# Performance work log

Hardware: AMD Instinct MI355X
Metric: run time of the kernel (lower is better)

The kernel has to match this reference:

```python
import jax, jax.numpy as jnp
import numpy as np

N = 8192      # atoms
F = 133       # atom feature length
H = 256       # hidden_size
MF = 200      # mol feature length
RH = 512      # readout_hidden_size
DEPTH = 3
N_RO = 2      # readout_num_hidden_layers
DEG = 32      # avg degree of random graph


def setup_inputs() -> dict:
    key = jax.random.key(0)
    ks = jax.random.split(key, 16)
    sc = 0.05
    adjacency_matrix = (jax.random.uniform(ks[0], (N, N)) < (DEG / N)).astype(jnp.float32)
    atom_feature_matrix = jax.random.normal(ks[1], (N, F), jnp.float32)
    molecule_features_vector = jax.random.normal(ks[2], (MF,), jnp.float32)
    return {
        "adjacency_matrix": adjacency_matrix,
        "atom_feature_matrix": atom_feature_matrix,
        "molecule_features_vector": molecule_features_vector,
        "W_in": jax.random.normal(ks[3], (F, H), jnp.float32) * sc,
        "b_in": jnp.zeros((H,), jnp.float32),
        "W_att": jax.random.normal(ks[4], (2 * H,), jnp.float32) * sc,
        "b_att": jnp.zeros((), jnp.float32),
        "W_node": jax.random.normal(ks[5], (DEPTH, H, H), jnp.float32) * sc,
        "b_node": jnp.zeros((DEPTH, H), jnp.float32),
        "W_ro_in": jax.random.normal(ks[6], (H + MF, RH), jnp.float32) * sc,
        "b_ro_in": jnp.zeros((RH,), jnp.float32),
        "W_ro_hid": jax.random.normal(ks[7], (N_RO, RH, RH), jnp.float32) * sc,
        "b_ro_hid": jnp.zeros((N_RO, RH), jnp.float32),
        "W_out": jax.random.normal(ks[8], (RH,), jnp.float32) * sc,
        "b_out": jnp.zeros((), jnp.float32),
    }


def reference(adjacency_matrix, atom_feature_matrix, molecule_features_vector,
              W_in, b_in, W_att, b_att, W_node, b_node,
              W_ro_in, b_ro_in, W_ro_hid, b_ro_hid, W_out, b_out):
    # input node-level linear
    h = atom_feature_matrix @ W_in + b_in                     # [N, H]
    wa_nei, wa_self = W_att[:H], W_att[H:]                    # concat([neighbor, self]) ordering
    for d in range(DEPTH):
        # attention score[i, j] = sigmoid(w_nei . h_j + w_self . h_i + b)
        s_nei = h @ wa_nei                                    # [N]
        s_self = h @ wa_self                                  # [N]
        att = jax.nn.sigmoid(s_self[:, None] + s_nei[None, :] + b_att)  # [N, N]
        # adjacency is binary: zeros stay zero, nonzeros get scaled by sigmoid score
        h = (adjacency_matrix * att) @ h                      # sum aggregation, [N, H]
        h = jax.nn.relu(h @ W_node[d] + b_node[d])
    # readout: sum over atoms, concat mol features
    g = jnp.sum(h, axis=0)                                    # [H]
    g = jnp.concatenate([g, molecule_features_vector])        # [H + MF]
    g = jax.nn.relu(g @ W_ro_in + b_ro_in)
    for d in range(N_RO):
        g = jax.nn.relu(g @ W_ro_hid[d] + b_ro_hid[d])
    return g @ W_out + b_out                                  # scalar
```

## Files before the change

### kernel.cpp

```cpp
#include <hip/hip_runtime.h>
#include <hip/hip_bf16.h>
#include <math.h>

#define N 8192
#define F 133
#define FP 136
#define H 256
#define MF 200
#define RH 512
#define MAXDEG 128

typedef unsigned short bfu;

static __device__ __forceinline__ bfu f2bf(float f) {
    unsigned u = __builtin_bit_cast(unsigned, f);
    u = (u + 0x7fff + ((u >> 16) & 1)) >> 16;
    return (bfu)u;
}
static __device__ __forceinline__ float bf2f(bfu b) {
    unsigned u = (unsigned)b << 16;
    return __builtin_bit_cast(float, u);
}

__global__ __launch_bounds__(256) void k_front(
    const float4* __restrict__ A4, int* __restrict__ cnt, int* __restrict__ colidx,
    const float* __restrict__ X, const float* __restrict__ Win,
    const float* __restrict__ bin, const float* __restrict__ Watt,
    bfu* __restrict__ hb, float* __restrict__ snei, float* __restrict__ sself,
    float* __restrict__ zbuf) {
    const int t = threadIdx.x;
    const int b = blockIdx.x;
    if (b == 2304) {
        for (int i = t; i < 1792; i += 256) zbuf[i] = 0.f;
        return;
    }
    if (b >= 256) {
        const int lane = t & 63;
        const int row = (b - 256) * 4 + (t >> 6);
        const float4* rowp = A4 + (size_t)row * (N / 4);
        unsigned w4[4];
#pragma unroll 1
        for (int c = 0; c < 4; ++c) {
            float4 v[8];
#pragma unroll
            for (int j = 0; j < 8; ++j) v[j] = rowp[c * 512 + j * 64 + lane];
            unsigned m = 0;
#pragma unroll
            for (int j = 0; j < 8; ++j) {
                const float* vp = &v[j].x;
#pragma unroll
                for (int q = 0; q < 4; ++q)
                    m |= (vp[q] != 0.0f) ? (1u << (j * 4 + q)) : 0u;
            }
            w4[c] = m;
        }
        int tl = __popc(w4[0]) + __popc(w4[1]) + __popc(w4[2]) + __popc(w4[3]);
        int inc = tl;
#pragma unroll
        for (int d = 1; d < 64; d <<= 1) {
            int nb = __shfl_up(inc, d);
            if (lane >= d) inc += nb;
        }
        int o = inc - tl;
        if (lane == 63) cnt[row] = inc < MAXDEG ? inc : MAXDEG;
        int* rowout = colidx + row * MAXDEG;
#pragma unroll
        for (int c = 0; c < 4; ++c) {
            unsigned m = w4[c];
            const int base = c * 2048 + lane * 4;
            while (m) {
                int p = __ffs(m) - 1;
                m &= m - 1;
                if (o < MAXDEG) rowout[o] = base + ((p >> 2) << 8) + (p & 3);
                ++o;
            }
        }
        return;
    }
    __shared__ float xs[32][FP];
    __shared__ float sredN[32][4];
    __shared__ float sredS[32][4];
    const int row0 = b * 32;
    for (int i = t; i < 32 * F; i += 256) {
        int r = i / F, f = i - r * F;
        xs[r][f] = X[(row0 + r) * F + f];
    }
    __syncthreads();
    float acc[32];
#pragma unroll
    for (int r = 0; r < 32; ++r) acc[r] = 0.f;
    for (int f = 0; f < 132; f += 4) {
        float w0 = Win[(f + 0) * H + t];
        float w1 = Win[(f + 1) * H + t];
        float w2 = Win[(f + 2) * H + t];
        float w3 = Win[(f + 3) * H + t];
#pragma unroll
        for (int r = 0; r < 32; ++r) {
            float4 xv = *reinterpret_cast<const float4*>(&xs[r][f]);
            acc[r] = fmaf(xv.x, w0, acc[r]);
            acc[r] = fmaf(xv.y, w1, acc[r]);
            acc[r] = fmaf(xv.z, w2, acc[r]);
            acc[r] = fmaf(xv.w, w3, acc[r]);
        }
    }
    {
        float w0 = Win[132 * H + t];
#pragma unroll
        for (int r = 0; r < 32; ++r) acc[r] = fmaf(xs[r][132], w0, acc[r]);
    }
    const float bb = bin[t];
    const float wan = Watt[t];
    const float was = Watt[H + t];
    const int wv = t >> 6, ln = t & 63;
#pragma unroll
    for (int r = 0; r < 32; ++r) {
        float v = acc[r] + bb;
        hb[(row0 + r) * H + t] = f2bf(v);
        float pn = v * wan;
        float ps = v * was;
        for (int off = 32; off > 0; off >>= 1) {
            pn += __shfl_down(pn, off);
            ps += __shfl_down(ps, off);
        }
        if (ln == 0) { sredN[r][wv] = pn; sredS[r][wv] = ps; }
    }
    __syncthreads();
    if (t < 32)
        snei[row0 + t] = (sredN[t][0] + sredN[t][1]) + (sredN[t][2] + sredN[t][3]);
    else if (t < 64) {
        int r = t - 32;
        sself[row0 + r] = (sredS[r][0] + sredS[r][1]) + (sredS[r][2] + sredS[r][3]);
    }
}

template <bool LAST>
__global__ __launch_bounds__(512, 2) void k_depth(
    const bfu* __restrict__ hin, bfu* __restrict__ hout,
    const int* __restrict__ cnt, const int* __restrict__ colidx,
    const float* __restrict__ snei_in, const float* __restrict__ sself_in,
    float* __restrict__ snei_out, float* __restrict__ sself_out,
    const float* __restrict__ Wn, const float* __restrict__ bn,
    const float* __restrict__ Watt, const float* __restrict__ b_att,
    float* __restrict__ gsum) {
    __shared__ float hs[32][260];
    __shared__ float uni[8192];
    __shared__ float sred[8 * 256];
    __shared__ float sselfL[32];
    __shared__ int   ncnt[32];
    const int t = threadIdx.x;
    const int w = t >> 6, l = t & 63;
    const int c0 = l << 2;
    const int R0 = blockIdx.x * 32;
    float* wls = uni;
    unsigned short* jls = (unsigned short*)(uni + 4096);

    if (t < 32) { ncnt[t] = cnt[R0 + t]; sselfL[t] = sself_in[R0 + t] + b_att[0]; }
    __syncthreads();
#pragma unroll
    for (int rep = 0; rep < 8; ++rep) {
        int idx = t + rep * 512;
        int r = idx >> 7, k = idx & 127;
        if (k < ncnt[r]) {
            int j = colidx[(R0 + r) * MAXDEG + k];
            jls[idx] = (unsigned short)j;
            wls[idx] = 1.f / (1.f + __expf(-(sselfL[r] + snei_in[j])));
        }
    }
    __syncthreads();
#define GSTEP(u, sx, sy, sz, sw)                                                  \
    { int ju = (int)jls[r * 128 + k + u]; float wv = wls[r * 128 + k + u];        \
      ushort4 hv = *reinterpret_cast<const ushort4*>(&hin[ju * 256 + c0]);        \
      sx = fmaf(wv, bf2f(hv.x), sx); sy = fmaf(wv, bf2f(hv.y), sy);               \
      sz = fmaf(wv, bf2f(hv.z), sz); sw = fmaf(wv, bf2f(hv.w), sw); }
#pragma unroll 1
    for (int rr = 0; rr < 4; ++rr) {
        const int r = w * 4 + rr;
        const int n = ncnt[r];
        float x0=0,y0=0,z0=0,w0=0, x1=0,y1=0,z1=0,w1=0;
        float x2=0,y2=0,z2=0,w2=0, x3=0,y3=0,z3=0,w3=0;
        float x4=0,y4=0,z4=0,w4=0, x5=0,y5=0,z5=0,w5=0;
        float x6=0,y6=0,z6=0,w6=0, x7=0,y7=0,z7=0,w7=0;
        int k = 0;
        for (; k + 8 <= n; k += 8) {
            GSTEP(0,x0,y0,z0,w0) GSTEP(1,x1,y1,z1,w1)
            GSTEP(2,x2,y2,z2,w2) GSTEP(3,x3,y3,z3,w3)
            GSTEP(4,x4,y4,z4,w4) GSTEP(5,x5,y5,z5,w5)
            GSTEP(6,x6,y6,z6,w6) GSTEP(7,x7,y7,z7,w7)
        }
        for (; k < n; ++k) { GSTEP(0,x0,y0,z0,w0) }
        float4 st;
        st.x = ((x0+x1)+(x2+x3)) + ((x4+x5)+(x6+x7));
        st.y = ((y0+y1)+(y2+y3)) + ((y4+y5)+(y6+y7));
        st.z = ((z0+z1)+(z2+z3)) + ((z4+z5)+(z6+z7));
        st.w = ((w0+w1)+(w2+w3)) + ((w4+w5)+(w6+w7));
        *reinterpret_cast<float4*>(&hs[r][c0]) = st;
    }
#undef GSTEP
    __syncthreads();

    float* Ws = uni;
    float acc[4][4];
#pragma unroll
    for (int i = 0; i < 4; ++i)
#pragma unroll
        for (int j = 0; j < 4; ++j) acc[i][j] = 0.f;
#pragma unroll 1
    for (int k0 = 0; k0 < 8; ++k0) {
        if (k0) __syncthreads();
#pragma unroll
        for (int j = 0; j < 4; ++j) {
            int idx = j * 512 + t;
            int kr = idx >> 6;
            int nc = (idx & 63) << 2;
            *reinterpret_cast<float4*>(&Ws[kr * 256 + nc]) =
                *reinterpret_cast<const float4*>(&Wn[(k0 * 32 + kr) * 256 + nc]);
        }
        __syncthreads();
#pragma unroll
        for (int k4 = 0; k4 < 8; ++k4) {
            float4 a0 = *reinterpret_cast<const float4*>(&hs[w * 4 + 0][k0 * 32 + k4 * 4]);
            float4 a1 = *reinterpret_cast<const float4*>(&hs[w * 4 + 1][k0 * 32 + k4 * 4]);
            float4 a2 = *reinterpret_cast<const float4*>(&hs[w * 4 + 2][k0 * 32 + k4 * 4]);
            float4 a3 = *reinterpret_cast<const float4*>(&hs[w * 4 + 3][k0 * 32 + k4 * 4]);
            const float* p0 = &a0.x;
            const float* p1 = &a1.x;
            const float* p2 = &a2.x;
            const float* p3 = &a3.x;
#pragma unroll
            for (int ki = 0; ki < 4; ++ki) {
                float4 wv = *reinterpret_cast<const float4*>(&Ws[(k4 * 4 + ki) * 256 + c0]);
                float aa0 = p0[ki], aa1 = p1[ki], aa2 = p2[ki], aa3 = p3[ki];
                acc[0][0] = fmaf(aa0, wv.x, acc[0][0]); acc[0][1] = fmaf(aa0, wv.y, acc[0][1]);
                acc[0][2] = fmaf(aa0, wv.z, acc[0][2]); acc[0][3] = fmaf(aa0, wv.w, acc[0][3]);
                acc[1][0] = fmaf(aa1, wv.x, acc[1][0]); acc[1][1] = fmaf(aa1, wv.y, acc[1][1]);
                acc[1][2] = fmaf(aa1, wv.z, acc[1][2]); acc[1][3] = fmaf(aa1, wv.w, acc[1][3]);
                acc[2][0] = fmaf(aa2, wv.x, acc[2][0]); acc[2][1] = fmaf(aa2, wv.y, acc[2][1]);
                acc[2][2] = fmaf(aa2, wv.z, acc[2][2]); acc[2][3] = fmaf(aa2, wv.w, acc[2][3]);
                acc[3][0] = fmaf(aa3, wv.x, acc[3][0]); acc[3][1] = fmaf(aa3, wv.y, acc[3][1]);
                acc[3][2] = fmaf(aa3, wv.z, acc[3][2]); acc[3][3] = fmaf(aa3, wv.w, acc[3][3]);
            }
        }
    }

    const float4 bv = *reinterpret_cast<const float4*>(&bn[c0]);
    float4 wanv, wasv;
    if (!LAST) {
        wanv = *reinterpret_cast<const float4*>(&Watt[c0]);
        wasv = *reinterpret_cast<const float4*>(&Watt[H + c0]);
    }
    float cs[4] = {0.f, 0.f, 0.f, 0.f};
#pragma unroll
    for (int i = 0; i < 4; ++i) {
        float v0 = acc[i][0] + bv.x; v0 = v0 > 0.f ? v0 : 0.f;
        float v1 = acc[i][1] + bv.y; v1 = v1 > 0.f ? v1 : 0.f;
        float v2 = acc[i][2] + bv.z; v2 = v2 > 0.f ? v2 : 0.f;
        float v3 = acc[i][3] + bv.w; v3 = v3 > 0.f ? v3 : 0.f;
        if (!LAST) {
            ushort4 o; o.x = f2bf(v0); o.y = f2bf(v1); o.z = f2bf(v2); o.w = f2bf(v3);
            *reinterpret_cast<ushort4*>(&hout[(R0 + w * 4 + i) * H + c0]) = o;
            float pn = v0 * wanv.x + v1 * wanv.y + v2 * wanv.z + v3 * wanv.w;
            float ps = v0 * wasv.x + v1 * wasv.y + v2 * wasv.z + v3 * wasv.w;
#pragma unroll
            for (int off = 32; off > 0; off >>= 1) {
                pn += __shfl_xor(pn, off);
                ps += __shfl_xor(ps, off);
            }
            if (l == 0) {
                snei_out[R0 + w * 4 + i] = pn;
                sself_out[R0 + w * 4 + i] = ps;
            }
        } else {
            cs[0] += v0; cs[1] += v1; cs[2] += v2; cs[3] += v3;
        }
    }
    if (LAST) {
#pragma unroll
        for (int j = 0; j < 4; ++j) sred[w * 256 + c0 + j] = cs[j];
        __syncthreads();
        if (t < 256) {
            float s = 0.f;
#pragma unroll
            for (int q = 0; q < 8; ++q) s += sred[q * 256 + t];
            atomicAdd(&gsum[t], s);
        }
    }
}

template <int MODE>
__global__ __launch_bounds__(256) void k_t(const float* __restrict__ xsrc,
                                           const float* __restrict__ bp,
                                           const float* __restrict__ mol,
                                           const float* __restrict__ W,
                                           float* __restrict__ pout) {
    const int K = (MODE == 0) ? (H + MF) : RH;
    const int KW = K / 8;
    const int lo = blockIdx.y * KW;
    __shared__ float xin[64];
    __shared__ float red[256];
    const int t = threadIdx.x;
    if (t < KW) {
        int k = lo + t;
        float xv;
        if (MODE == 0) xv = (k < H) ? xsrc[k] : mol[k - H];
        else {
            float p = xsrc[k] + bp[k];
            xv = p > 0.f ? p : 0.f;
        }
        xin[t] = xv;
    }
    __syncthreads();
    const int o = blockIdx.x * 64 + (t & 63);
    const int kg = t >> 6;
    float acc = 0.f;
    for (int k = kg; k < KW; k += 4)
        acc = fmaf(xin[k], W[(lo + k) * RH + o], acc);
    red[t] = acc;
    __syncthreads();
    if (t < 64) {
        float s = red[t] + red[t + 64] + red[t + 128] + red[t + 192];
        atomicAdd(&pout[o], s);
    }
}

__global__ __launch_bounds__(512) void k_fin(const float* __restrict__ g3p,
                                             const float* __restrict__ b3,
                                             const float* __restrict__ Wo,
                                             const float* __restrict__ bo,
                                             float* __restrict__ out) {
    __shared__ float red[512];
    const int t = threadIdx.x;
    float v = g3p[t] + b3[t];
    v = v > 0.f ? v : 0.f;
    red[t] = v * Wo[t];
    __syncthreads();
    for (int s = 256; s > 0; s >>= 1) {
        if (t < s) red[t] += red[t + s];
        __syncthreads();
    }
    if (t == 0) out[0] = red[0] + bo[0];
}

extern "C" void kernel_launch(void* const* d_in, const int* in_sizes, int n_in,
                              void* d_out, int out_size, void* d_ws, size_t ws_size,
                              hipStream_t stream) {
    const float* A        = (const float*)d_in[0];
    const float* X        = (const float*)d_in[1];
    const float* mol      = (const float*)d_in[2];
    const float* W_in     = (const float*)d_in[3];
    const float* b_in     = (const float*)d_in[4];
    const float* W_att    = (const float*)d_in[5];
    const float* b_att    = (const float*)d_in[6];
    const float* W_node   = (const float*)d_in[7];
    const float* b_node   = (const float*)d_in[8];
    const float* W_ro_in  = (const float*)d_in[9];
    const float* b_ro_in  = (const float*)d_in[10];
    const float* W_ro_hid = (const float*)d_in[11];
    const float* b_ro_hid = (const float*)d_in[12];
    const float* W_out    = (const float*)d_in[13];
    const float* b_out    = (const float*)d_in[14];

    char* ws = (char*)d_ws;
    bfu*   hb_a   = (bfu*)  (ws);
    bfu*   hb_b   = (bfu*)  (ws + 4194304);
    int*   colidx = (int*)  (ws + 8388608);
    int*   cnt    = (int*)  (ws + 12582912);
    float* s0n    = (float*)(ws + 12615680);
    float* s0s    = (float*)(ws + 12648448);
    float* s1n    = (float*)(ws + 12681216);
    float* s1s    = (float*)(ws + 12713984);
    float* zbuf   = (float*)(ws + 12746752);
    float* gsum   = zbuf;
    float* g1p    = zbuf + 256;
    float* g2p    = zbuf + 768;
    float* g3p    = zbuf + 1280;

    k_front<<<2305, 256, 0, stream>>>((const float4*)A, cnt, colidx,
                                      X, W_in, b_in, W_att, hb_a, s0n, s0s, zbuf);
    k_depth<false><<<256, 512, 0, stream>>>(
        hb_a, hb_b, cnt, colidx, s0n, s0s, s1n, s1s,
        W_node + 0 * H * H, b_node + 0 * H, W_att, b_att, nullptr);
    k_depth<false><<<256, 512, 0, stream>>>(
        hb_b, hb_a, cnt, colidx, s1n, s1s, s0n, s0s,
        W_node + 1 * H * H, b_node + 1 * H, W_att, b_att, nullptr);
    k_depth<true><<<256, 512, 0, stream>>>(
        hb_a, nullptr, cnt, colidx, s0n, s0s, nullptr, nullptr,
        W_node + 2 * H * H, b_node + 2 * H, W_att, b_att, gsum);
    k_t<0><<<dim3(8, 8), 256, 0, stream>>>(gsum, nullptr, mol, W_ro_in, g1p);
    k_t<1><<<dim3(8, 8), 256, 0, stream>>>(g1p, b_ro_in, nullptr, W_ro_hid, g2p);
    k_t<1><<<dim3(8, 8), 256, 0, stream>>>(g2p, b_ro_hid, nullptr,
                                           W_ro_hid + RH * RH, g3p);
    k_fin<<<1, 512, 0, stream>>>(g3p, b_ro_hid + RH, W_out, b_out, (float*)d_out);
}
```

Measured before the change: 208.7 us.

## Fuse readout MLP launches into single-block tail kernel with double-buffered weights

Replaces the three split-K readout matvec kernels and the final dot-product kernel with one 1024-thread single-block kernel that streams each weight matrix through shared memory in double-buffered 16-row chunks. This removes three kernel launches and the atomic partial-sum buffers along with their zeroing. In exchange, about 1.3 MB of readout weights is read by a single compute unit instead of 64 blocks, so the tail may become bandwidth-bound on one CU.

Measured after the change: 283.8 us. +36.0%, slower.

```diff
diff --git a/kernel.cpp b/kernel.cpp
--- a/kernel.cpp
+++ b/kernel.cpp
@@ -27,11 +27,11 @@
     const float* __restrict__ X, const float* __restrict__ Win,
     const float* __restrict__ bin, const float* __restrict__ Watt,
     bfu* __restrict__ hb, float* __restrict__ snei, float* __restrict__ sself,
-    float* __restrict__ zbuf) {
+    float* __restrict__ gsum) {
     const int t = threadIdx.x;
     const int b = blockIdx.x;
     if (b == 2304) {
-        for (int i = t; i < 1792; i += 256) zbuf[i] = 0.f;
+        if (t < 256) gsum[t] = 0.f;
         return;
     }
     if (b >= 256) {
@@ -286,54 +286,78 @@
     }
 }
 
-template <int MODE>
-__global__ __launch_bounds__(256) void k_t(const float* __restrict__ xsrc,
-                                           const float* __restrict__ bp,
-                                           const float* __restrict__ mol,
-                                           const float* __restrict__ W,
-                                           float* __restrict__ pout) {
-    const int K = (MODE == 0) ? (H + MF) : RH;
-    const int KW = K / 8;
-    const int lo = blockIdx.y * KW;
-    __shared__ float xin[64];
-    __shared__ float red[256];
+#define TCH 16
+__global__ __launch_bounds__(1024) void k_tail(
+    const float* __restrict__ gsum, const float* __restrict__ mol,
+    const float* __restrict__ W1, const float* __restrict__ b1,
+    const float* __restrict__ Wh, const float* __restrict__ bh,
+    const float* __restrict__ Wo, const float* __restrict__ bo,
+    float* __restrict__ out) {
+    __shared__ float Ws[2][TCH * 512];
+    __shared__ float xa[512];
+    __shared__ float red[1024];
     const int t = threadIdx.x;
-    if (t < KW) {
-        int k = lo + t;
-        float xv;
-        if (MODE == 0) xv = (k < H) ? xsrc[k] : mol[k - H];
-        else {
-            float p = xsrc[k] + bp[k];
-            xv = p > 0.f ? p : 0.f;
-        }
-        xin[t] = xv;
-    }
-    __syncthreads();
-    const int o = blockIdx.x * 64 + (t & 63);
-    const int kg = t >> 6;
-    float acc = 0.f;
-    for (int k = kg; k < KW; k += 4)
-        acc = fmaf(xin[k], W[(lo + k) * RH + o], acc);
-    red[t] = acc;
-    __syncthreads();
-    if (t < 64) {
-        float s = red[t] + red[t + 64] + red[t + 128] + red[t + 192];
-        atomicAdd(&pout[o], s);
-    }
-}
-
-__global__ __launch_bounds__(512) void k_fin(const float* __restrict__ g3p,
-                                             const float* __restrict__ b3,
-                                             const float* __restrict__ Wo,
-                                             const float* __restrict__ bo,
-                                             float* __restrict__ out) {
-    __shared__ float red[512];
-    const int t = threadIdx.x;
-    float v = g3p[t] + b3[t];
-    v = v > 0.f ? v : 0.f;
-    red[t] = v * Wo[t];
-    __syncthreads();
-    for (int s = 256; s > 0; s >>= 1) {
+    const int o = t & 511;
+    const int kg = t >> 9;
+    if (t < H) xa[t] = gsum[t];
+    else if (t < H + MF) xa[t] = mol[t - H];
+    else if (t < 512) xa[t] = 0.f;
+    __syncthreads();
+#pragma unroll 1
+    for (int L = 0; L < 3; ++L) {
+        const float* W = (L == 0) ? W1 : ((L == 1) ? Wh : (Wh + RH * RH));
+        const int K = (L == 0) ? (H + MF) : RH;
+        const int nc = (K + TCH - 1) / TCH;
+        {
+            const float4* gp = (const float4*)W;
+            float4* ds = (float4*)&Ws[0][0];
+            ds[t] = gp[t];
+            ds[t + 1024] = gp[t + 1024];
+        }
+        __syncthreads();
+        float acc = 0.f;
+#pragma unroll 1
+        for (int c = 0; c < nc; ++c) {
+            const int cur = c & 1;
+            const bool have = (c + 1) < nc;
+            const int nkc = have ? ((K - (c + 1) * TCH) < TCH ? (K - (c + 1) * TCH) : TCH) : 0;
+            const int nf4 = nkc * 128;
+            float4 pf0, pf1;
+            bool g0 = false, g1 = false;
+            if (have) {
+                const float4* gp = (const float4*)(W + (c + 1) * TCH * 512);
+                g0 = (t < nf4);
+                g1 = (t + 1024 < nf4);
+                if (g0) pf0 = gp[t];
+                if (g1) pf1 = gp[t + 1024];
+            }
+            const int kc = (K - c * TCH) < TCH ? (K - c * TCH) : TCH;
+            const int kh = kc >> 1;
+            const int kbeg = kg ? kh : 0;
+            const int kend = kg ? kc : kh;
+            const float* wsp = &Ws[cur][0];
+#pragma unroll 8
+            for (int k = kbeg; k < kend; ++k)
+                acc = fmaf(xa[c * TCH + k], wsp[k * 512 + o], acc);
+            if (have) {
+                float4* ds = (float4*)&Ws[1 - cur][0];
+                if (g0) ds[t] = pf0;
+                if (g1) ds[t + 1024] = pf1;
+            }
+            __syncthreads();
+        }
+        red[t] = acc;
+        __syncthreads();
+        if (t < 512) {
+            float bb = (L == 0) ? b1[t] : ((L == 1) ? bh[t] : bh[RH + t]);
+            float v = red[t] + red[t + 512] + bb;
+            xa[t] = v > 0.f ? v : 0.f;
+        }
+        __syncthreads();
+    }
+    red[t] = (t < 512) ? xa[t] * Wo[t] : 0.f;
+    __syncthreads();
+    for (int s = 512; s > 0; s >>= 1) {
         if (t < s) red[t] += red[t + s];
         __syncthreads();
     }
@@ -368,14 +392,10 @@
     float* s0s    = (float*)(ws + 12648448);
     float* s1n    = (float*)(ws + 12681216);
     float* s1s    = (float*)(ws + 12713984);
-    float* zbuf   = (float*)(ws + 12746752);
-    float* gsum   = zbuf;
-    float* g1p    = zbuf + 256;
-    float* g2p    = zbuf + 768;
-    float* g3p    = zbuf + 1280;
+    float* gsum   = (float*)(ws + 12746752);
 
     k_front<<<2305, 256, 0, stream>>>((const float4*)A, cnt, colidx,
-                                      X, W_in, b_in, W_att, hb_a, s0n, s0s, zbuf);
+                                      X, W_in, b_in, W_att, hb_a, s0n, s0s, gsum);
     k_depth<false><<<256, 512, 0, stream>>>(
         hb_a, hb_b, cnt, colidx, s0n, s0s, s1n, s1s,
         W_node + 0 * H * H, b_node + 0 * H, W_att, b_att, nullptr);
@@ -385,9 +405,6 @@
     k_depth<true><<<256, 512, 0, stream>>>(
         hb_a, nullptr, cnt, colidx, s0n, s0s, nullptr, nullptr,
         W_node + 2 * H * H, b_node + 2 * H, W_att, b_att, gsum);
-    k_t<0><<<dim3(8, 8), 256, 0, stream>>>(gsum, nullptr, mol, W_ro_in, g1p);
-    k_t<1><<<dim3(8, 8), 256, 0, stream>>>(g1p, b_ro_in, nullptr, W_ro_hid, g2p);
-    k_t<1><<<dim3(8, 8), 256, 0, stream>>>(g2p, b_ro_hid, nullptr,
-                                           W_ro_hid + RH * RH, g3p);
-    k_fin<<<1, 512, 0, stream>>>(g3p, b_ro_hid + RH, W_out, b_out, (float*)d_out);
-}
+    k_tail<<<1, 1024, 0, stream>>>(gsum, mol, W_ro_in, b_ro_in, W_ro_hid, b_ro_hid,
+                                   W_out, b_out, (float*)d_out);
+}
```

## Shrink k_depth LDS with bf16 staging and fuse final readout kernel

Applied to the files above, without the earlier changes.

Stores the aggregated rows and the attention weights in shared memory as bf16 instead of fp32, and halves the W_node staging tile to 16 rows, so k_depth uses much less LDS. The launch bound minimum blocks goes from 2 to 6 to allow more resident workgroups. Separately, the last readout matvec and the final dot product are fused into one kernel using a last-block counter. This adds bf16 rounding on the intermediate aggregation and doubles the number of barrier-separated weight-load rounds, and the tighter launch bound may force register spills.

Result: slower. 233.9 us (+12.1%).

```diff
diff --git a/kernel.cpp b/kernel.cpp
--- a/kernel.cpp
+++ b/kernel.cpp
@@ -31,7 +31,7 @@
     const int t = threadIdx.x;
     const int b = blockIdx.x;
     if (b == 2304) {
-        for (int i = t; i < 1792; i += 256) zbuf[i] = 0.f;
+        for (int i = t; i < 1800; i += 256) zbuf[i] = 0.f;
         return;
     }
     if (b >= 256) {
@@ -134,7 +134,7 @@
 }
 
 template <bool LAST>
-__global__ __launch_bounds__(512, 2) void k_depth(
+__global__ __launch_bounds__(512, 6) void k_depth(
     const bfu* __restrict__ hin, bfu* __restrict__ hout,
     const int* __restrict__ cnt, const int* __restrict__ colidx,
     const float* __restrict__ snei_in, const float* __restrict__ sself_in,
@@ -142,8 +142,8 @@
     const float* __restrict__ Wn, const float* __restrict__ bn,
     const float* __restrict__ Watt, const float* __restrict__ b_att,
     float* __restrict__ gsum) {
-    __shared__ float hs[32][260];
-    __shared__ float uni[8192];
+    __shared__ bfu   hsb[32][264];
+    __shared__ float uni[4096];
     __shared__ float sred[8 * 256];
     __shared__ float sselfL[32];
     __shared__ int   ncnt[32];
@@ -151,8 +151,8 @@
     const int w = t >> 6, l = t & 63;
     const int c0 = l << 2;
     const int R0 = blockIdx.x * 32;
-    float* wls = uni;
-    unsigned short* jls = (unsigned short*)(uni + 4096);
+    bfu* wlsb = (bfu*)uni;
+    unsigned short* jls = ((unsigned short*)uni) + 4096;
 
     if (t < 32) { ncnt[t] = cnt[R0 + t]; sselfL[t] = sself_in[R0 + t] + b_att[0]; }
     __syncthreads();
@@ -163,12 +163,12 @@
         if (k < ncnt[r]) {
             int j = colidx[(R0 + r) * MAXDEG + k];
             jls[idx] = (unsigned short)j;
-            wls[idx] = 1.f / (1.f + __expf(-(sselfL[r] + snei_in[j])));
+            wlsb[idx] = f2bf(1.f / (1.f + __expf(-(sselfL[r] + snei_in[j]))));
         }
     }
     __syncthreads();
 #define GSTEP(u, sx, sy, sz, sw)                                                  \
-    { int ju = (int)jls[r * 128 + k + u]; float wv = wls[r * 128 + k + u];        \
+    { int ju = (int)jls[r * 128 + k + u]; float wv = bf2f(wlsb[r * 128 + k + u]); \
       ushort4 hv = *reinterpret_cast<const ushort4*>(&hin[ju * 256 + c0]);        \
       sx = fmaf(wv, bf2f(hv.x), sx); sy = fmaf(wv, bf2f(hv.y), sy);               \
       sz = fmaf(wv, bf2f(hv.z), sz); sw = fmaf(wv, bf2f(hv.w), sw); }
@@ -188,12 +188,12 @@
             GSTEP(6,x6,y6,z6,w6) GSTEP(7,x7,y7,z7,w7)
         }
         for (; k < n; ++k) { GSTEP(0,x0,y0,z0,w0) }
-        float4 st;
-        st.x = ((x0+x1)+(x2+x3)) + ((x4+x5)+(x6+x7));
-        st.y = ((y0+y1)+(y2+y3)) + ((y4+y5)+(y6+y7));
-        st.z = ((z0+z1)+(z2+z3)) + ((z4+z5)+(z6+z7));
-        st.w = ((w0+w1)+(w2+w3)) + ((w4+w5)+(w6+w7));
-        *reinterpret_cast<float4*>(&hs[r][c0]) = st;
+        ushort4 st;
+        st.x = f2bf(((x0+x1)+(x2+x3)) + ((x4+x5)+(x6+x7)));
+        st.y = f2bf(((y0+y1)+(y2+y3)) + ((y4+y5)+(y6+y7)));
+        st.z = f2bf(((z0+z1)+(z2+z3)) + ((z4+z5)+(z6+z7)));
+        st.w = f2bf(((w0+w1)+(w2+w3)) + ((w4+w5)+(w6+w7)));
+        *reinterpret_cast<ushort4*>(&hsb[r][c0]) = st;
     }
 #undef GSTEP
     __syncthreads();
@@ -205,27 +205,27 @@
 #pragma unroll
         for (int j = 0; j < 4; ++j) acc[i][j] = 0.f;
 #pragma unroll 1
-    for (int k0 = 0; k0 < 8; ++k0) {
+    for (int k0 = 0; k0 < 16; ++k0) {
         if (k0) __syncthreads();
 #pragma unroll
-        for (int j = 0; j < 4; ++j) {
+        for (int j = 0; j < 2; ++j) {
             int idx = j * 512 + t;
             int kr = idx >> 6;
             int nc = (idx & 63) << 2;
             *reinterpret_cast<float4*>(&Ws[kr * 256 + nc]) =
-                *reinterpret_cast<const float4*>(&Wn[(k0 * 32 + kr) * 256 + nc]);
+                *reinterpret_cast<const float4*>(&Wn[(k0 * 16 + kr) * 256 + nc]);
         }
         __syncthreads();
 #pragma unroll
-        for (int k4 = 0; k4 < 8; ++k4) {
-            float4 a0 = *reinterpret_cast<const float4*>(&hs[w * 4 + 0][k0 * 32 + k4 * 4]);
-            float4 a1 = *reinterpret_cast<const float4*>(&hs[w * 4 + 1][k0 * 32 + k4 * 4]);
-            float4 a2 = *reinterpret_cast<const float4*>(&hs[w * 4 + 2][k0 * 32 + k4 * 4]);
-            float4 a3 = *reinterpret_cast<const float4*>(&hs[w * 4 + 3][k0 * 32 + k4 * 4]);
-            const float* p0 = &a0.x;
-            const float* p1 = &a1.x;
-            const float* p2 = &a2.x;
-            const float* p3 = &a3.x;
+        for (int k4 = 0; k4 < 4; ++k4) {
+            ushort4 a0 = *reinterpret_cast<const ushort4*>(&hsb[w * 4 + 0][k0 * 16 + k4 * 4]);
+            ushort4 a1 = *reinterpret_cast<const ushort4*>(&hsb[w * 4 + 1][k0 * 16 + k4 * 4]);
+            ushort4 a2 = *reinterpret_cast<const ushort4*>(&hsb[w * 4 + 2][k0 * 16 + k4 * 4]);
+            ushort4 a3 = *reinterpret_cast<const ushort4*>(&hsb[w * 4 + 3][k0 * 16 + k4 * 4]);
+            float p0[4] = {bf2f(a0.x), bf2f(a0.y), bf2f(a0.z), bf2f(a0.w)};
+            float p1[4] = {bf2f(a1.x), bf2f(a1.y), bf2f(a1.z), bf2f(a1.w)};
+            float p2[4] = {bf2f(a2.x), bf2f(a2.y), bf2f(a2.z), bf2f(a2.w)};
+            float p3[4] = {bf2f(a3.x), bf2f(a3.y), bf2f(a3.z), bf2f(a3.w)};
 #pragma unroll
             for (int ki = 0; ki < 4; ++ki) {
                 float4 wv = *reinterpret_cast<const float4*>(&Ws[(k4 * 4 + ki) * 256 + c0]);
@@ -322,18 +322,49 @@
     }
 }
 
-__global__ __launch_bounds__(512) void k_fin(const float* __restrict__ g3p,
-                                             const float* __restrict__ b3,
-                                             const float* __restrict__ Wo,
-                                             const float* __restrict__ bo,
-                                             float* __restrict__ out) {
-    __shared__ float red[512];
+__global__ __launch_bounds__(256) void k_t_fin(const float* __restrict__ xsrc,
+                                               const float* __restrict__ bp,
+                                               const float* __restrict__ W,
+                                               float* __restrict__ pout,
+                                               const float* __restrict__ b3,
+                                               const float* __restrict__ Wo,
+                                               const float* __restrict__ bo,
+                                               int* __restrict__ done,
+                                               float* __restrict__ out) {
+    const int KW = RH / 8;
+    const int lo = blockIdx.y * KW;
+    __shared__ float xin[64];
+    __shared__ float red[256];
+    __shared__ int lastb;
     const int t = threadIdx.x;
-    float v = g3p[t] + b3[t];
-    v = v > 0.f ? v : 0.f;
-    red[t] = v * Wo[t];
-    __syncthreads();
-    for (int s = 256; s > 0; s >>= 1) {
+    if (t < KW) {
+        float p = xsrc[lo + t] + bp[lo + t];
+        xin[t] = p > 0.f ? p : 0.f;
+    }
+    __syncthreads();
+    const int o = blockIdx.x * 64 + (t & 63);
+    const int kg = t >> 6;
+    float acc = 0.f;
+    for (int k = kg; k < KW; k += 4)
+        acc = fmaf(xin[k], W[(lo + k) * RH + o], acc);
+    red[t] = acc;
+    __syncthreads();
+    if (t < 64) {
+        float s = red[t] + red[t + 64] + red[t + 128] + red[t + 192];
+        atomicAdd(&pout[o], s);
+    }
+    __threadfence();
+    __syncthreads();
+    if (t == 0) lastb = (atomicAdd(done, 1) == 63) ? 1 : 0;
+    __syncthreads();
+    if (!lastb) return;
+    float v0 = atomicAdd(&pout[t], 0.f) + b3[t];
+    float v1 = atomicAdd(&pout[t + 256], 0.f) + b3[t + 256];
+    v0 = v0 > 0.f ? v0 : 0.f;
+    v1 = v1 > 0.f ? v1 : 0.f;
+    red[t] = v0 * Wo[t] + v1 * Wo[t + 256];
+    __syncthreads();
+    for (int s = 128; s > 0; s >>= 1) {
         if (t < s) red[t] += red[t + s];
         __syncthreads();
     }
@@ -373,6 +404,7 @@
     float* g1p    = zbuf + 256;
     float* g2p    = zbuf + 768;
     float* g3p    = zbuf + 1280;
+    int*   done   = (int*)(zbuf + 1792);
 
     k_front<<<2305, 256, 0, stream>>>((const float4*)A, cnt, colidx,
                                       X, W_in, b_in, W_att, hb_a, s0n, s0s, zbuf);
@@ -387,7 +419,7 @@
         W_node + 2 * H * H, b_node + 2 * H, W_att, b_att, gsum);
     k_t<0><<<dim3(8, 8), 256, 0, stream>>>(gsum, nullptr, mol, W_ro_in, g1p);
     k_t<1><<<dim3(8, 8), 256, 0, stream>>>(g1p, b_ro_in, nullptr, W_ro_hid, g2p);
-    k_t<1><<<dim3(8, 8), 256, 0, stream>>>(g2p, b_ro_hid, nullptr,
-                                           W_ro_hid + RH * RH, g3p);
-    k_fin<<<1, 512, 0, stream>>>(g3p, b_ro_hid + RH, W_out, b_out, (float*)d_out);
-}
+    k_t_fin<<<dim3(8, 8), 256, 0, stream>>>(g2p, b_ro_hid, W_ro_hid + RH * RH, g3p,
+                                            b_ro_hid + RH, W_out, b_out, done,
+                                            (float*)d_out);
+}
```

## Fuse depth layers and readout MLP into one cooperative persistent kernel

Applied to the files above, without the earlier changes.

Replaces the three per-depth kernels and four readout kernels with a single cooperative kernel that loops over depths and uses grid-wide syncs between phases. The readout layers run on 64 blocks with grid syncs, and the final reduction uses a last-block-done counter. The aim is to remove launch overhead and inter-kernel gaps for the small readout work. The cost is grid.sync barriers, and the cooperative launch requires all 256 blocks to be co-resident.

Result: slower. 387.9 us (+85.8%).

```diff
diff --git a/kernel.cpp b/kernel.cpp
--- a/kernel.cpp
+++ b/kernel.cpp
@@ -1,6 +1,9 @@
 #include <hip/hip_runtime.h>
 #include <hip/hip_bf16.h>
+#include <hip/hip_cooperative_groups.h>
 #include <math.h>
+
+namespace cg = cooperative_groups;
 
 #define N 8192
 #define F 133
@@ -31,7 +34,7 @@
     const int t = threadIdx.x;
     const int b = blockIdx.x;
     if (b == 2304) {
-        for (int i = t; i < 1792; i += 256) zbuf[i] = 0.f;
+        for (int i = t; i < 1800; i += 256) zbuf[i] = 0.f;
         return;
     }
     if (b >= 256) {
@@ -133,211 +136,262 @@
     }
 }
 
-template <bool LAST>
-__global__ __launch_bounds__(512, 2) void k_depth(
-    const bfu* __restrict__ hin, bfu* __restrict__ hout,
+__global__ __launch_bounds__(512, 2) void k_main(
+    bfu* __restrict__ hba, bfu* __restrict__ hbb,
     const int* __restrict__ cnt, const int* __restrict__ colidx,
-    const float* __restrict__ snei_in, const float* __restrict__ sself_in,
-    float* __restrict__ snei_out, float* __restrict__ sself_out,
-    const float* __restrict__ Wn, const float* __restrict__ bn,
+    float* __restrict__ s0n, float* __restrict__ s0s,
+    float* __restrict__ s1n, float* __restrict__ s1s,
+    const float* __restrict__ Wnode, const float* __restrict__ bnode,
     const float* __restrict__ Watt, const float* __restrict__ b_att,
-    float* __restrict__ gsum) {
+    float* __restrict__ gsum, const float* __restrict__ mol,
+    const float* __restrict__ W1, const float* __restrict__ b1,
+    const float* __restrict__ Wh, const float* __restrict__ bh,
+    const float* __restrict__ Wo, const float* __restrict__ bo,
+    float* __restrict__ g1p, float* __restrict__ g2p, float* __restrict__ g3p,
+    int* __restrict__ done, float* __restrict__ out) {
+    cg::grid_group grid = cg::this_grid();
     __shared__ float hs[32][260];
     __shared__ float uni[8192];
-    __shared__ float sred[8 * 256];
+    __shared__ float sred[2048];
     __shared__ float sselfL[32];
     __shared__ int   ncnt[32];
+    __shared__ int   lastb;
     const int t = threadIdx.x;
     const int w = t >> 6, l = t & 63;
     const int c0 = l << 2;
-    const int R0 = blockIdx.x * 32;
+    const int b = blockIdx.x;
+    const int R0 = b * 32;
     float* wls = uni;
     unsigned short* jls = (unsigned short*)(uni + 4096);
 
-    if (t < 32) { ncnt[t] = cnt[R0 + t]; sselfL[t] = sself_in[R0 + t] + b_att[0]; }
-    __syncthreads();
-#pragma unroll
-    for (int rep = 0; rep < 8; ++rep) {
-        int idx = t + rep * 512;
-        int r = idx >> 7, k = idx & 127;
-        if (k < ncnt[r]) {
-            int j = colidx[(R0 + r) * MAXDEG + k];
-            jls[idx] = (unsigned short)j;
-            wls[idx] = 1.f / (1.f + __expf(-(sselfL[r] + snei_in[j])));
-        }
-    }
-    __syncthreads();
+#pragma unroll 1
+    for (int d = 0; d < 3; ++d) {
+        const bool last = (d == 2);
+        const bfu* hin = (d == 1) ? hbb : hba;
+        bfu* hout = (d == 0) ? hbb : hba;
+        const float* sni = (d == 1) ? s1n : s0n;
+        const float* ssi = (d == 1) ? s1s : s0s;
+        float* sno = (d == 0) ? s1n : s0n;
+        float* sso = (d == 0) ? s1s : s0s;
+        const float* Wn = Wnode + d * H * H;
+        const float* bn = bnode + d * H;
+
+        if (t < 32) { ncnt[t] = cnt[R0 + t]; sselfL[t] = ssi[R0 + t] + b_att[0]; }
+        __syncthreads();
+#pragma unroll
+        for (int rep = 0; rep < 8; ++rep) {
+            int idx = t + rep * 512;
+            int r = idx >> 7, k = idx & 127;
+            if (k < ncnt[r]) {
+                int j = colidx[(R0 + r) * MAXDEG + k];
+                jls[idx] = (unsigned short)j;
+                wls[idx] = 1.f / (1.f + __expf(-(sselfL[r] + sni[j])));
+            }
+        }
+        __syncthreads();
 #define GSTEP(u, sx, sy, sz, sw)                                                  \
-    { int ju = (int)jls[r * 128 + k + u]; float wv = wls[r * 128 + k + u];        \
-      ushort4 hv = *reinterpret_cast<const ushort4*>(&hin[ju * 256 + c0]);        \
-      sx = fmaf(wv, bf2f(hv.x), sx); sy = fmaf(wv, bf2f(hv.y), sy);               \
-      sz = fmaf(wv, bf2f(hv.z), sz); sw = fmaf(wv, bf2f(hv.w), sw); }
+        { int ju = (int)jls[r * 128 + k + u]; float wv = wls[r * 128 + k + u];    \
+          ushort4 hv = *reinterpret_cast<const ushort4*>(&hin[ju * 256 + c0]);    \
+          sx = fmaf(wv, bf2f(hv.x), sx); sy = fmaf(wv, bf2f(hv.y), sy);           \
+          sz = fmaf(wv, bf2f(hv.z), sz); sw = fmaf(wv, bf2f(hv.w), sw); }
 #pragma unroll 1
-    for (int rr = 0; rr < 4; ++rr) {
-        const int r = w * 4 + rr;
-        const int n = ncnt[r];
-        float x0=0,y0=0,z0=0,w0=0, x1=0,y1=0,z1=0,w1=0;
-        float x2=0,y2=0,z2=0,w2=0, x3=0,y3=0,z3=0,w3=0;
-        float x4=0,y4=0,z4=0,w4=0, x5=0,y5=0,z5=0,w5=0;
-        float x6=0,y6=0,z6=0,w6=0, x7=0,y7=0,z7=0,w7=0;
-        int k = 0;
-        for (; k + 8 <= n; k += 8) {
-            GSTEP(0,x0,y0,z0,w0) GSTEP(1,x1,y1,z1,w1)
-            GSTEP(2,x2,y2,z2,w2) GSTEP(3,x3,y3,z3,w3)
-            GSTEP(4,x4,y4,z4,w4) GSTEP(5,x5,y5,z5,w5)
-            GSTEP(6,x6,y6,z6,w6) GSTEP(7,x7,y7,z7,w7)
-        }
-        for (; k < n; ++k) { GSTEP(0,x0,y0,z0,w0) }
-        float4 st;
-        st.x = ((x0+x1)+(x2+x3)) + ((x4+x5)+(x6+x7));
-        st.y = ((y0+y1)+(y2+y3)) + ((y4+y5)+(y6+y7));
-        st.z = ((z0+z1)+(z2+z3)) + ((z4+z5)+(z6+z7));
-        st.w = ((w0+w1)+(w2+w3)) + ((w4+w5)+(w6+w7));
-        *reinterpret_cast<float4*>(&hs[r][c0]) = st;
-    }
+        for (int rr = 0; rr < 4; ++rr) {
+            const int r = w * 4 + rr;
+            const int n = ncnt[r];
+            float x0=0,y0=0,z0=0,w0=0, x1=0,y1=0,z1=0,w1=0;
+            float x2=0,y2=0,z2=0,w2=0, x3=0,y3=0,z3=0,w3=0;
+            float x4=0,y4=0,z4=0,w4=0, x5=0,y5=0,z5=0,w5=0;
+            float x6=0,y6=0,z6=0,w6=0, x7=0,y7=0,z7=0,w7=0;
+            int k = 0;
+            for (; k + 8 <= n; k += 8) {
+                GSTEP(0,x0,y0,z0,w0) GSTEP(1,x1,y1,z1,w1)
+                GSTEP(2,x2,y2,z2,w2) GSTEP(3,x3,y3,z3,w3)
+                GSTEP(4,x4,y4,z4,w4) GSTEP(5,x5,y5,z5,w5)
+                GSTEP(6,x6,y6,z6,w6) GSTEP(7,x7,y7,z7,w7)
+            }
+            for (; k < n; ++k) { GSTEP(0,x0,y0,z0,w0) }
+            float4 st;
+            st.x = ((x0+x1)+(x2+x3)) + ((x4+x5)+(x6+x7));
+            st.y = ((y0+y1)+(y2+y3)) + ((y4+y5)+(y6+y7));
+            st.z = ((z0+z1)+(z2+z3)) + ((z4+z5)+(z6+z7));
+            st.w = ((w0+w1)+(w2+w3)) + ((w4+w5)+(w6+w7));
+            *reinterpret_cast<float4*>(&hs[r][c0]) = st;
+        }
 #undef GSTEP
-    __syncthreads();
-
-    float* Ws = uni;
-    float acc[4][4];
-#pragma unroll
-    for (int i = 0; i < 4; ++i)
-#pragma unroll
-        for (int j = 0; j < 4; ++j) acc[i][j] = 0.f;
+        __syncthreads();
+
+        float* Ws = uni;
+        float acc[4][4];
+#pragma unroll
+        for (int i = 0; i < 4; ++i)
+#pragma unroll
+            for (int j = 0; j < 4; ++j) acc[i][j] = 0.f;
 #pragma unroll 1
-    for (int k0 = 0; k0 < 8; ++k0) {
-        if (k0) __syncthreads();
-#pragma unroll
-        for (int j = 0; j < 4; ++j) {
-            int idx = j * 512 + t;
-            int kr = idx >> 6;
-            int nc = (idx & 63) << 2;
-            *reinterpret_cast<float4*>(&Ws[kr * 256 + nc]) =
-                *reinterpret_cast<const float4*>(&Wn[(k0 * 32 + kr) * 256 + nc]);
-        }
-        __syncthreads();
-#pragma unroll
-        for (int k4 = 0; k4 < 8; ++k4) {
-            float4 a0 = *reinterpret_cast<const float4*>(&hs[w * 4 + 0][k0 * 32 + k4 * 4]);
-            float4 a1 = *reinterpret_cast<const float4*>(&hs[w * 4 + 1][k0 * 32 + k4 * 4]);
-            float4 a2 = *reinterpret_cast<const float4*>(&hs[w * 4 + 2][k0 * 32 + k4 * 4]);
-            float4 a3 = *reinterpret_cast<const float4*>(&hs[w * 4 + 3][k0 * 32 + k4 * 4]);
-            const float* p0 = &a0.x;
-            const float* p1 = &a1.x;
-            const float* p2 = &a2.x;
-            const float* p3 = &a3.x;
-#pragma unroll
-            for (int ki = 0; ki < 4; ++ki) {
-                float4 wv = *reinterpret_cast<const float4*>(&Ws[(k4 * 4 + ki) * 256 + c0]);
-                float aa0 = p0[ki], aa1 = p1[ki], aa2 = p2[ki], aa3 = p3[ki];
-                acc[0][0] = fmaf(aa0, wv.x, acc[0][0]); acc[0][1] = fmaf(aa0, wv.y, acc[0][1]);
-                acc[0][2] = fmaf(aa0, wv.z, acc[0][2]); acc[0][3] = fmaf(aa0, wv.w, acc[0][3]);
-                acc[1][0] = fmaf(aa1, wv.x, acc[1][0]); acc[1][1] = fmaf(aa1, wv.y, acc[1][1]);
-                acc[1][2] = fmaf(aa1, wv.z, acc[1][2]); acc[1][3] = fmaf(aa1, wv.w, acc[1][3]);
-                acc[2][0] = fmaf(aa2, wv.x, acc[2][0]); acc[2][1] = fmaf(aa2, wv.y, acc[2][1]);
-                acc[2][2] = fmaf(aa2, wv.z, acc[2][2]); acc[2][3] = fmaf(aa2, wv.w, acc[2][3]);
-                acc[3][0] = fmaf(aa3, wv.x, acc[3][0]); acc[3][1] = fmaf(aa3, wv.y, acc[3][1]);
-                acc[3][2] = fmaf(aa3, wv.z, acc[3][2]); acc[3][3] = fmaf(aa3, wv.w, acc[3][3]);
-            }
-        }
-    }
-
-    const float4 bv = *reinterpret_cast<const float4*>(&bn[c0]);
-    float4 wanv, wasv;
-    if (!LAST) {
-        wanv = *reinterpret_cast<const float4*>(&Watt[c0]);
-        wasv = *reinterpret_cast<const float4*>(&Watt[H + c0]);
-    }
-    float cs[4] = {0.f, 0.f, 0.f, 0.f};
-#pragma unroll
-    for (int i = 0; i < 4; ++i) {
-        float v0 = acc[i][0] + bv.x; v0 = v0 > 0.f ? v0 : 0.f;
-        float v1 = acc[i][1] + bv.y; v1 = v1 > 0.f ? v1 : 0.f;
-        float v2 = acc[i][2] + bv.z; v2 = v2 > 0.f ? v2 : 0.f;
-        float v3 = acc[i][3] + bv.w; v3 = v3 > 0.f ? v3 : 0.f;
-        if (!LAST) {
-            ushort4 o; o.x = f2bf(v0); o.y = f2bf(v1); o.z = f2bf(v2); o.w = f2bf(v3);
-            *reinterpret_cast<ushort4*>(&hout[(R0 + w * 4 + i) * H + c0]) = o;
-            float pn = v0 * wanv.x + v1 * wanv.y + v2 * wanv.z + v3 * wanv.w;
-            float ps = v0 * wasv.x + v1 * wasv.y + v2 * wasv.z + v3 * wasv.w;
-#pragma unroll
-            for (int off = 32; off > 0; off >>= 1) {
-                pn += __shfl_xor(pn, off);
-                ps += __shfl_xor(ps, off);
-            }
-            if (l == 0) {
-                snei_out[R0 + w * 4 + i] = pn;
-                sself_out[R0 + w * 4 + i] = ps;
-            }
-        } else {
-            cs[0] += v0; cs[1] += v1; cs[2] += v2; cs[3] += v3;
-        }
-    }
-    if (LAST) {
-#pragma unroll
-        for (int j = 0; j < 4; ++j) sred[w * 256 + c0 + j] = cs[j];
-        __syncthreads();
-        if (t < 256) {
+        for (int k0 = 0; k0 < 8; ++k0) {
+            if (k0) __syncthreads();
+#pragma unroll
+            for (int j = 0; j < 4; ++j) {
+                int idx = j * 512 + t;
+                int kr = idx >> 6;
+                int nc = (idx & 63) << 2;
+                *reinterpret_cast<float4*>(&Ws[kr * 256 + nc]) =
+                    *reinterpret_cast<const float4*>(&Wn[(k0 * 32 + kr) * 256 + nc]);
+            }
+            __syncthreads();
+#pragma unroll
+            for (int k4 = 0; k4 < 8; ++k4) {
+                float4 a0 = *reinterpret_cast<const float4*>(&hs[w * 4 + 0][k0 * 32 + k4 * 4]);
+                float4 a1 = *reinterpret_cast<const float4*>(&hs[w * 4 + 1][k0 * 32 + k4 * 4]);
+                float4 a2 = *reinterpret_cast<const float4*>(&hs[w * 4 + 2][k0 * 32 + k4 * 4]);
+                float4 a3 = *reinterpret_cast<const float4*>(&hs[w * 4 + 3][k0 * 32 + k4 * 4]);
+                const float* p0 = &a0.x;
+                const float* p1 = &a1.x;
+                const float* p2 = &a2.x;
+                const float* p3 = &a3.x;
+#pragma unroll
+                for (int ki = 0; ki < 4; ++ki) {
+                    float4 wv = *reinterpret_cast<const float4*>(&Ws[(k4 * 4 + ki) * 256 + c0]);
+                    float aa0 = p0[ki], aa1 = p1[ki], aa2 = p2[ki], aa3 = p3[ki];
+                    acc[0][0] = fmaf(aa0, wv.x, acc[0][0]); acc[0][1] = fmaf(aa0, wv.y, acc[0][1]);
+                    acc[0][2] = fmaf(aa0, wv.z, acc[0][2]); acc[0][3] = fmaf(aa0, wv.w, acc[0][3]);
+                    acc[1][0] = fmaf(aa1, wv.x, acc[1][0]); acc[1][1] = fmaf(aa1, wv.y, acc[1][1]);
+                    acc[1][2] = fmaf(aa1, wv.z, acc[1][2]); acc[1][3] = fmaf(aa1, wv.w, acc[1][3]);
+                    acc[2][0] = fmaf(aa2, wv.x, acc[2][0]); acc[2][1] = fmaf(aa2, wv.y, acc[2][1]);
+                    acc[2][2] = fmaf(aa2, wv.z, acc[2][2]); acc[2][3] = fmaf(aa2, wv.w, acc[2][3]);
+                    acc[3][0] = fmaf(aa3, wv.x, acc[3][0]); acc[3][1] = fmaf(aa3, wv.y, acc[3][1]);
+                    acc[3][2] = fmaf(aa3, wv.z, acc[3][2]); acc[3][3] = fmaf(aa3, wv.w, acc[3][3]);
+                }
+            }
+        }
+
+        const float4 bv = *reinterpret_cast<const float4*>(&bn[c0]);
+        float4 wanv, wasv;
+        if (!last) {
+            wanv = *reinterpret_cast<const float4*>(&Watt[c0]);
+            wasv = *reinterpret_cast<const float4*>(&Watt[H + c0]);
+        }
+        float cs[4] = {0.f, 0.f, 0.f, 0.f};
+#pragma unroll
+        for (int i = 0; i < 4; ++i) {
+            float v0 = acc[i][0] + bv.x; v0 = v0 > 0.f ? v0 : 0.f;
+            float v1 = acc[i][1] + bv.y; v1 = v1 > 0.f ? v1 : 0.f;
+            float v2 = acc[i][2] + bv.z; v2 = v2 > 0.f ? v2 : 0.f;
+            float v3 = acc[i][3] + bv.w; v3 = v3 > 0.f ? v3 : 0.f;
+            if (!last) {
+                ushort4 o; o.x = f2bf(v0); o.y = f2bf(v1); o.z = f2bf(v2); o.w = f2bf(v3);
+                *reinterpret_cast<ushort4*>(&hout[(R0 + w * 4 + i) * H + c0]) = o;
+                float pn = v0 * wanv.x + v1 * wanv.y + v2 * wanv.z + v3 * wanv.w;
+                float ps = v0 * wasv.x + v1 * wasv.y + v2 * wasv.z + v3 * wasv.w;
+#pragma unroll
+                for (int off = 32; off > 0; off >>= 1) {
+                    pn += __shfl_xor(pn, off);
+                    ps += __shfl_xor(ps, off);
+                }
+                if (l == 0) {
+                    sno[R0 + w * 4 + i] = pn;
+                    sso[R0 + w * 4 + i] = ps;
+                }
+            } else {
+                cs[0] += v0; cs[1] += v1; cs[2] += v2; cs[3] += v3;
+            }
+        }
+        if (last) {
+#pragma unroll
+            for (int j = 0; j < 4; ++j) sred[w * 256 + c0 + j] = cs[j];
+            __syncthreads();
+            if (t < 256) {
+                float s = 0.f;
+#pragma unroll
+                for (int q = 0; q < 8; ++q) s += sred[q * 256 + t];
+                atomicAdd(&gsum[t], s);
+            }
+        }
+        grid.sync();
+    }
+
+    float* xin = uni;
+    float* red = sred;
+    if (b < 64) {
+        const int KW = 57;
+        const int og = b >> 3, lo = (b & 7) * KW;
+        if (t < KW) {
+            int k = lo + t;
+            xin[t] = (k < H) ? atomicAdd(&gsum[k], 0.f) : mol[k - H];
+        }
+        __syncthreads();
+        const int o = og * 64 + (t & 63);
+        const int kg = t >> 6;
+        float acc = 0.f;
+        for (int k = kg; k < KW; k += 8) acc = fmaf(xin[k], W1[(lo + k) * RH + o], acc);
+        red[t] = acc;
+        __syncthreads();
+        if (t < 64) {
             float s = 0.f;
 #pragma unroll
-            for (int q = 0; q < 8; ++q) s += sred[q * 256 + t];
-            atomicAdd(&gsum[t], s);
-        }
-    }
-}
-
-template <int MODE>
-__global__ __launch_bounds__(256) void k_t(const float* __restrict__ xsrc,
-                                           const float* __restrict__ bp,
-                                           const float* __restrict__ mol,
-                                           const float* __restrict__ W,
-                                           float* __restrict__ pout) {
-    const int K = (MODE == 0) ? (H + MF) : RH;
-    const int KW = K / 8;
-    const int lo = blockIdx.y * KW;
-    __shared__ float xin[64];
-    __shared__ float red[256];
-    const int t = threadIdx.x;
-    if (t < KW) {
-        int k = lo + t;
-        float xv;
-        if (MODE == 0) xv = (k < H) ? xsrc[k] : mol[k - H];
-        else {
-            float p = xsrc[k] + bp[k];
-            xv = p > 0.f ? p : 0.f;
-        }
-        xin[t] = xv;
-    }
-    __syncthreads();
-    const int o = blockIdx.x * 64 + (t & 63);
-    const int kg = t >> 6;
-    float acc = 0.f;
-    for (int k = kg; k < KW; k += 4)
-        acc = fmaf(xin[k], W[(lo + k) * RH + o], acc);
-    red[t] = acc;
-    __syncthreads();
-    if (t < 64) {
-        float s = red[t] + red[t + 64] + red[t + 128] + red[t + 192];
-        atomicAdd(&pout[o], s);
-    }
-}
-
-__global__ __launch_bounds__(512) void k_fin(const float* __restrict__ g3p,
-                                             const float* __restrict__ b3,
-                                             const float* __restrict__ Wo,
-                                             const float* __restrict__ bo,
-                                             float* __restrict__ out) {
-    __shared__ float red[512];
-    const int t = threadIdx.x;
-    float v = g3p[t] + b3[t];
-    v = v > 0.f ? v : 0.f;
-    red[t] = v * Wo[t];
-    __syncthreads();
-    for (int s = 256; s > 0; s >>= 1) {
-        if (t < s) red[t] += red[t + s];
-        __syncthreads();
-    }
-    if (t == 0) out[0] = red[0] + bo[0];
+            for (int q = 0; q < 8; ++q) s += red[t + 64 * q];
+            atomicAdd(&g1p[o], s);
+        }
+    }
+    grid.sync();
+    if (b < 64) {
+        const int KW = 64;
+        const int og = b >> 3, lo = (b & 7) * KW;
+        if (t < KW) {
+            float p = atomicAdd(&g1p[lo + t], 0.f) + b1[lo + t];
+            xin[t] = p > 0.f ? p : 0.f;
+        }
+        __syncthreads();
+        const int o = og * 64 + (t & 63);
+        const int kg = t >> 6;
+        float acc = 0.f;
+        for (int k = kg; k < KW; k += 8) acc = fmaf(xin[k], Wh[(lo + k) * RH + o], acc);
+        red[t] = acc;
+        __syncthreads();
+        if (t < 64) {
+            float s = 0.f;
+#pragma unroll
+            for (int q = 0; q < 8; ++q) s += red[t + 64 * q];
+            atomicAdd(&g2p[o], s);
+        }
+    }
+    grid.sync();
+    if (b < 64) {
+        const float* W3 = Wh + RH * RH;
+        const int KW = 64;
+        const int og = b >> 3, lo = (b & 7) * KW;
+        if (t < KW) {
+            float p = atomicAdd(&g2p[lo + t], 0.f) + bh[lo + t];
+            xin[t] = p > 0.f ? p : 0.f;
+        }
+        __syncthreads();
+        const int o = og * 64 + (t & 63);
+        const int kg = t >> 6;
+        float acc = 0.f;
+        for (int k = kg; k < KW; k += 8) acc = fmaf(xin[k], W3[(lo + k) * RH + o], acc);
+        red[t] = acc;
+        __syncthreads();
+        if (t < 64) {
+            float s = 0.f;
+#pragma unroll
+            for (int q = 0; q < 8; ++q) s += red[t + 64 * q];
+            atomicAdd(&g3p[o], s);
+        }
+        __threadfence();
+        __syncthreads();
+        if (t == 0) lastb = (atomicAdd(done, 1) == 63) ? 1 : 0;
+        __syncthreads();
+        if (lastb) {
+            float v = atomicAdd(&g3p[t], 0.f) + bh[RH + t];
+            v = v > 0.f ? v : 0.f;
+            red[t] = v * Wo[t];
+            __syncthreads();
+            for (int s = 256; s > 0; s >>= 1) {
+                if (t < s) red[t] += red[t + s];
+                __syncthreads();
+            }
+            if (t == 0) out[0] = red[0] + bo[0];
+        }
+    }
 }
 
 extern "C" void kernel_launch(void* const* d_in, const int* in_sizes, int n_in,
@@ -373,21 +427,19 @@
     float* g1p    = zbuf + 256;
     float* g2p    = zbuf + 768;
     float* g3p    = zbuf + 1280;
+    int*   done   = (int*)(zbuf + 1792);
+    float* out_f  = (float*)d_out;
 
     k_front<<<2305, 256, 0, stream>>>((const float4*)A, cnt, colidx,
                                       X, W_in, b_in, W_att, hb_a, s0n, s0s, zbuf);
-    k_depth<false><<<256, 512, 0, stream>>>(
-        hb_a, hb_b, cnt, colidx, s0n, s0s, s1n, s1s,
-        W_node + 0 * H * H, b_node + 0 * H, W_att, b_att, nullptr);
-    k_depth<false><<<256, 512, 0, stream>>>(
-        hb_b, hb_a, cnt, colidx, s1n, s1s, s0n, s0s,
-        W_node + 1 * H * H, b_node + 1 * H, W_att, b_att, nullptr);
-    k_depth<true><<<256, 512, 0, stream>>>(
-        hb_a, nullptr, cnt, colidx, s0n, s0s, nullptr, nullptr,
-        W_node + 2 * H * H, b_node + 2 * H, W_att, b_att, gsum);
-    k_t<0><<<dim3(8, 8), 256, 0, stream>>>(gsum, nullptr, mol, W_ro_in, g1p);
-    k_t<1><<<dim3(8, 8), 256, 0, stream>>>(g1p, b_ro_in, nullptr, W_ro_hid, g2p);
-    k_t<1><<<dim3(8, 8), 256, 0, stream>>>(g2p, b_ro_hid, nullptr,
-                                           W_ro_hid + RH * RH, g3p);
-    k_fin<<<1, 512, 0, stream>>>(g3p, b_ro_hid + RH, W_out, b_out, (float*)d_out);
+    void* args[] = {
+        (void*)&hb_a, (void*)&hb_b, (void*)&cnt, (void*)&colidx,
+        (void*)&s0n, (void*)&s0s, (void*)&s1n, (void*)&s1s,
+        (void*)&W_node, (void*)&b_node, (void*)&W_att, (void*)&b_att,
+        (void*)&gsum, (void*)&mol, (void*)&W_ro_in, (void*)&b_ro_in,
+        (void*)&W_ro_hid, (void*)&b_ro_hid, (void*)&W_out, (void*)&b_out,
+        (void*)&g1p, (void*)&g2p, (void*)&g3p, (void*)&done, (void*)&out_f};
+    hipError_t err = hipLaunchCooperativeKernel((void*)k_main, dim3(256), dim3(512),
+                                                args, 0, stream);
+    (void)err;
 }
```
